# Optimization experiments

Hardware: AMD Instinct MI355X
Metric: run time of the kernel (lower is better)

## Reference

```python
import jax, jax.numpy as jnp
import numpy as np


def setup_inputs() -> dict:
    key = jax.random.key(0)
    kx, kw, kb = jax.random.split(key, 3)
    x = jax.random.normal(kx, (4, 2048, 4096), dtype=jnp.float32)
    weight = jax.random.normal(kw, (4096, 4096), dtype=jnp.float32) * 0.02
    bias = jax.random.normal(kb, (4096,), dtype=jnp.float32) * 0.02
    return {"x": x, "weight": weight, "bias": bias}


def _binarize_except_outliers(w):
    # Outlier mask from global weight stats (computed from w itself; in torch it
    # is cached after the first call but the values are identical every step).
    mean = jnp.mean(w)
    std = jnp.std(w, ddof=1)  # torch.std default is the unbiased estimator
    lower = mean - 1.96 * std
    upper = mean + 1.96 * std
    outliers = (w < lower) | (w > upper)
    keep = (~outliers).astype(w.dtype)
    # scaling_factor in the torch code: w[~outliers].abs().mean(-1) on the
    # flattened masked-select -> a single SCALAR, detached from the graph.
    scale = jax.lax.stop_gradient(jnp.sum(jnp.abs(w) * keep) / jnp.sum(keep))
    # NOTE: the torch code assigns STE-sign values and then immediately
    # overwrites them with w * scale, so the effective math is:
    w_bin = jnp.where(outliers, w, w * scale)
    return w_bin


def reference(x, weight, bias):
    w_bin = _binarize_except_outliers(weight)  # [out, in]
    # F.linear(x, w, b) = x @ w.T + b
    return jnp.einsum("bsi,oi->bso", x, w_bin) + bias
```

## Files before the change

### kernel.cpp

```cpp
#include <hip/hip_runtime.h>
#include <hip/hip_bf16.h>
#include <math.h>

#define MDIM 8192
#define NDIM 4096
#define KDIM 4096
#define WELEMS 16777216
#define XELEMS 33554432

typedef __attribute__((ext_vector_type(8))) short bf16x8;
typedef __attribute__((ext_vector_type(4))) float f32x4;

__device__ __forceinline__ unsigned short f2bf(float f) {
  unsigned int u = __float_as_uint(f);
  u += 0x7fffu + ((u >> 16) & 1u);
  return (unsigned short)(u >> 16);
}

__device__ __forceinline__ void gload16(const void* g, void* l) {
  __builtin_amdgcn_global_load_lds(
      (const __attribute__((address_space(1))) void*)g,
      (__attribute__((address_space(3))) void*)l, 16, 0, 0);
}

template <int MODE>
__global__ __launch_bounds__(256)
void np_stage1(const float* __restrict__ w, float* __restrict__ C,
               float* __restrict__ C2, const float* __restrict__ scal) {
  __shared__ float ls[32], ls2[32];
  const int t = threadIdx.x;
  const int leaf = t >> 3, j = t & 7;
  const size_t base = (size_t)blockIdx.x * 4096 + leaf * 128 + j;
  float mean = 0.f, lower = 0.f, upper = 0.f;
  if (MODE == 1) mean = scal[0];
  if (MODE == 2) { lower = scal[1]; upper = scal[2]; }
  float r = 0.f, r2 = 0.f;
#pragma unroll
  for (int s = 0; s < 16; s++) {
    float v = w[base + s * 8];
    float tv, tv2 = 0.f;
    if (MODE == 0) tv = v;
    else if (MODE == 1) { float x = v - mean; tv = __fmul_rn(x, x); }
    else {
      bool keep = !(v < lower || v > upper);
      tv = keep ? fabsf(v) : 0.f;
      tv2 = keep ? 1.f : 0.f;
    }
    if (s == 0) { r = tv; r2 = tv2; } else { r += tv; r2 += tv2; }
  }
  r += __shfl_xor(r, 1); r += __shfl_xor(r, 2); r += __shfl_xor(r, 4);
  if (MODE == 2) { r2 += __shfl_xor(r2, 1); r2 += __shfl_xor(r2, 2); r2 += __shfl_xor(r2, 4); }
  if (j == 0) { ls[leaf] = r; if (MODE == 2) ls2[leaf] = r2; }
  __syncthreads();
  if (t == 0) {
    float tmp[32];
    for (int i = 0; i < 32; i++) tmp[i] = ls[i];
    for (int n = 32; n > 1; n >>= 1)
      for (int i = 0; i < n / 2; i++) tmp[i] = tmp[2 * i] + tmp[2 * i + 1];
    C[blockIdx.x] = tmp[0];
    if (MODE == 2) {
      for (int i = 0; i < 32; i++) tmp[i] = ls2[i];
      for (int n = 32; n > 1; n >>= 1)
        for (int i = 0; i < n / 2; i++) tmp[i] = tmp[2 * i] + tmp[2 * i + 1];
      C2[blockIdx.x] = tmp[0];
    }
  }
}

template <int MODE>
__global__ __launch_bounds__(256)
void np_stage2(const float* __restrict__ C, const float* __restrict__ C2,
               float* __restrict__ scal) {
  __shared__ float ls[256], ls2[256];
  const int t = threadIdx.x;
  {
    float v[16];
    for (int i = 0; i < 16; i++) v[i] = C[t * 16 + i];
    for (int n = 16; n > 1; n >>= 1)
      for (int i = 0; i < n / 2; i++) v[i] = v[2 * i] + v[2 * i + 1];
    ls[t] = v[0];
    if (MODE == 2) {
      for (int i = 0; i < 16; i++) v[i] = C2[t * 16 + i];
      for (int n = 16; n > 1; n >>= 1)
        for (int i = 0; i < n / 2; i++) v[i] = v[2 * i] + v[2 * i + 1];
      ls2[t] = v[0];
    }
  }
  __syncthreads();
  if (t == 0) {
    float tmp[256];
    for (int i = 0; i < 256; i++) tmp[i] = ls[i];
    for (int n = 256; n > 1; n >>= 1)
      for (int i = 0; i < n / 2; i++) tmp[i] = tmp[2 * i] + tmp[2 * i + 1];
    float S = tmp[0];
    if (MODE == 0) {
      scal[0] = S / 16777216.0f;
    } else if (MODE == 1) {
      float var = S / 16777215.0f;
      float sd = sqrtf(var);
      float mean = scal[0];
      scal[1] = mean - __fmul_rn(1.96f, sd);
      scal[2] = mean + __fmul_rn(1.96f, sd);
    } else {
      for (int i = 0; i < 256; i++) tmp[i] = ls2[i];
      for (int n = 256; n > 1; n >>= 1)
        for (int i = 0; i < n / 2; i++) tmp[i] = tmp[2 * i] + tmp[2 * i + 1];
      scal[3] = S / tmp[0];
    }
  }
}

__device__ __forceinline__ void pack8(const float* __restrict__ p, unsigned short* dst,
                                      bool dobin, float lower, float upper, float scale) {
  float4 u = *(const float4*)p;
  float4 v = *(const float4*)(p + 4);
  float f[8] = {u.x, u.y, u.z, u.w, v.x, v.y, v.z, v.w};
  unsigned int r[4];
#pragma unroll
  for (int j = 0; j < 4; j++) {
    float a = f[2 * j], b = f[2 * j + 1];
    if (dobin) {
      bool oa = (a < lower) || (a > upper);
      bool ob = (b < lower) || (b > upper);
      a = oa ? a : __fmul_rn(a, scale);
      b = ob ? b : __fmul_rn(b, scale);
    }
    r[j] = (unsigned int)f2bf(a) | ((unsigned int)f2bf(b) << 16);
  }
  *(uint4*)dst = make_uint4(r[0], r[1], r[2], r[3]);
}

__global__ __launch_bounds__(256)
void convert_w(const float* __restrict__ w, unsigned short* __restrict__ wb,
               const float* __restrict__ scal) {
  float lower = scal[1], upper = scal[2], scale = scal[3];
  int tid = blockIdx.x * blockDim.x + threadIdx.x;
  int nth = gridDim.x * blockDim.x;
  int nc = WELEMS / 8;
  for (int i = tid; i < nc; i += nth)
    pack8(w + (size_t)i * 8, wb + (size_t)i * 8, true, lower, upper, scale);
}

__global__ __launch_bounds__(256)
void convert_x(const float* __restrict__ x, unsigned short* __restrict__ xb) {
  int tid = blockIdx.x * blockDim.x + threadIdx.x;
  int nth = gridDim.x * blockDim.x;
  int nc = XELEMS / 8;
  for (int i = tid; i < nc; i += nth)
    pack8(x + (size_t)i * 8, xb + (size_t)i * 8, false, 0.f, 0.f, 0.f);
}


#define VM(n) asm volatile("s_waitcnt vmcnt(" #n ")" ::: "memory")
#define PSYNC { asm volatile("" ::: "memory"); __builtin_amdgcn_s_barrier(); asm volatile("" ::: "memory"); }

#define RDA(slot, bufR, h) do { \
  slot[0][0] = *(const bf16x8*)&sA[bufR][wm][((2*(h)  )*16+fr)*64 + koo0]; \
  slot[0][1] = *(const bf16x8*)&sA[bufR][wm][((2*(h)  )*16+fr)*64 + koo1]; \
  slot[1][0] = *(const bf16x8*)&sA[bufR][wm][((2*(h)+1)*16+fr)*64 + koo0]; \
  slot[1][1] = *(const bf16x8*)&sA[bufR][wm][((2*(h)+1)*16+fr)*64 + koo1]; } while (0)

#define RDB2(slot, nf, bufR, bh) do { \
  slot[nf][0] = *(const bf16x8*)&sB[bufR][wnh][(wnq*64+(2*(bh)+(nf))*16+fr)*64 + koo0]; \
  slot[nf][1] = *(const bf16x8*)&sB[bufR][wnh][(wnq*64+(2*(bh)+(nf))*16+fr)*64 + koo1]; } while (0)

#define RDB4(slot, bufR, bh) do { RDB2(slot, 0, bufR, bh); RDB2(slot, 1, bufR, bh); } while (0)

#define MM8(AS, BSL, h, nh) do { \
  __builtin_amdgcn_s_setprio(1); \
  acc[2*(h)  ][2*(nh)  ] = __builtin_amdgcn_mfma_f32_16x16x32_bf16(AS[0][0], BSL[0][0], acc[2*(h)  ][2*(nh)  ], 0, 0, 0); \
  acc[2*(h)  ][2*(nh)+1] = __builtin_amdgcn_mfma_f32_16x16x32_bf16(AS[0][0], BSL[1][0], acc[2*(h)  ][2*(nh)+1], 0, 0, 0); \
  acc[2*(h)+1][2*(nh)  ] = __builtin_amdgcn_mfma_f32_16x16x32_bf16(AS[1][0], BSL[0][0], acc[2*(h)+1][2*(nh)  ], 0, 0, 0); \
  acc[2*(h)+1][2*(nh)+1] = __builtin_amdgcn_mfma_f32_16x16x32_bf16(AS[1][0], BSL[1][0], acc[2*(h)+1][2*(nh)+1], 0, 0, 0); \
  acc[2*(h)  ][2*(nh)  ] = __builtin_amdgcn_mfma_f32_16x16x32_bf16(AS[0][1], BSL[0][1], acc[2*(h)  ][2*(nh)  ], 0, 0, 0); \
  acc[2*(h)  ][2*(nh)+1] = __builtin_amdgcn_mfma_f32_16x16x32_bf16(AS[0][1], BSL[1][1], acc[2*(h)  ][2*(nh)+1], 0, 0, 0); \
  acc[2*(h)+1][2*(nh)  ] = __builtin_amdgcn_mfma_f32_16x16x32_bf16(AS[1][1], BSL[0][1], acc[2*(h)+1][2*(nh)  ], 0, 0, 0); \
  acc[2*(h)+1][2*(nh)+1] = __builtin_amdgcn_mfma_f32_16x16x32_bf16(AS[1][1], BSL[1][1], acc[2*(h)+1][2*(nh)+1], 0, 0, 0); \
  __builtin_amdgcn_s_setprio(0); } while (0)

#define STGA(buf, q, kadd) do { \
  gload16(xbp + aofA[0][q] + (kadd), &sA[buf][0][(q)*4096 + t8]); \
  gload16(xbp + aofA[1][q] + (kadd), &sA[buf][1][(q)*4096 + t8]); } while (0)
#define STGB(buf, h, kadd) do { \
  gload16(wbp + bofB[h][0] + (kadd), &sB[buf][h][t8]); \
  gload16(wbp + bofB[h][1] + (kadd), &sB[buf][h][4096 + t8]); } while (0)

#define TILE(BR, BW, BF, BS_, KADD) do { \
   PSYNC; RDB2(BS_, 0, BR, 1); STGA(BW, 0, KADD); MM8(aA, BF, 0, 0); \
   PSYNC; RDB2(BS_, 1, BR, 1); STGB(BW, 0, KADD); MM8(aB, BF, 1, 0); VM(4); \
   PSYNC; RDA(aC, BR, 2); STGB(BW, 1, KADD); MM8(aB, BS_, 1, 1); \
   PSYNC; RDA(aB, BR, 3); STGA(BW, 1, KADD); MM8(aA, BS_, 0, 1); \
   PSYNC; MM8(aC, BS_, 2, 1); VM(6); \
   PSYNC; RDA(aA, BW, 0); MM8(aB, BS_, 3, 1); VM(2); \
   PSYNC; MM8(aB, BF, 3, 0); RDB4(BS_, BW, 0); \
   PSYNC; MM8(aC, BF, 2, 0); RDA(aB, BW, 1); } while (0)

__global__ __launch_bounds__(512, 2)
void gemm256(const unsigned short* __restrict__ xbp, const unsigned short* __restrict__ wbp,
             const float* __restrict__ bias, float* __restrict__ out) {
  __shared__ unsigned short sA[2][2][8192];
  __shared__ unsigned short sB[2][2][8192];

  const int bid = blockIdx.x;
  const int swz = (bid & 7) * 64 + (bid >> 3);
  const int bm = swz >> 4, bn = swz & 15;

  const int t = threadIdx.x;
  const int lane = t & 63;
  const int wid = t >> 6;
  const int wm = wid >> 2, wn = wid & 3;
  const int wnh = wn >> 1, wnq = wn & 1;
  const int fr = lane & 15;
  const int ko = (lane >> 4) * 8;
  const int xr = (fr & 7) << 3;
  const int koo0 = ko ^ xr;
  const int koo1 = (32 + ko) ^ xr;

  const int t8 = t * 8;
  const int rl = t >> 3;
  const int cs = ((t & 7) * 8) ^ ((rl & 7) << 3);
  unsigned int aofA[2][2], bofB[2][2];
#pragma unroll
  for (int h = 0; h < 2; h++)
#pragma unroll
    for (int q = 0; q < 2; q++) {
      aofA[h][q] = (unsigned int)((bm * 256 + h * 128 + q * 64 + rl) * KDIM + cs);
      bofB[h][q] = (unsigned int)((bn * 256 + h * 128 + q * 64 + rl) * KDIM + cs);
    }

  f32x4 acc[8][4];
#pragma unroll
  for (int i = 0; i < 8; i++)
#pragma unroll
    for (int j = 0; j < 4; j++) acc[i][j] = {0.f, 0.f, 0.f, 0.f};

  bf16x8 aA[2][2], aB[2][2], aC[2][2], bs0[2][2], bs1[2][2];

  STGA(0, 0, 0); STGB(0, 0, 0); STGB(0, 1, 0); STGA(0, 1, 0);
  VM(2); PSYNC;
  RDA(aA, 0, 0); RDA(aB, 0, 1); RDB4(bs0, 0, 0);

  for (int it = 0; it < 31; ++it) {
    TILE(0, 1, bs0, bs1, 64);
    TILE(1, 0, bs1, bs0, 128);
#pragma unroll
    for (int h = 0; h < 2; h++)
#pragma unroll
      for (int q = 0; q < 2; q++) { aofA[h][q] += 128; bofB[h][q] += 128; }
  }
  TILE(0, 1, bs0, bs1, 64);
   PSYNC; RDB2(bs0, 0, 1, 1); MM8(aA, bs1, 0, 0);
   PSYNC; RDB2(bs0, 1, 1, 1); MM8(aB, bs1, 1, 0); VM(0);
   PSYNC; RDA(aC, 1, 2); MM8(aB, bs0, 1, 1);
   PSYNC; RDA(aB, 1, 3); MM8(aA, bs0, 0, 1);
   PSYNC; MM8(aC, bs0, 2, 1);
   PSYNC; MM8(aB, bs0, 3, 1);
   PSYNC; MM8(aB, bs1, 3, 0);
   PSYNC; MM8(aC, bs1, 2, 0);

#pragma unroll
  for (int nn = 0; nn < 4; ++nn) {
    const int col = bn * 256 + wn * 64 + nn * 16 + (lane & 15);
    const float bv = bias[col];
#pragma unroll
    for (int m = 0; m < 8; ++m) {
      const int row0 = bm * 256 + wm * 128 + m * 16 + (lane >> 4) * 4;
#pragma unroll
      for (int q = 0; q < 4; ++q)
        out[(size_t)(row0 + q) * NDIM + col] = acc[m][nn][q] + bv;
    }
  }
}

template <bool A_BF16, bool B_BF16>
__global__ __launch_bounds__(256)
void gemm_bt(const void* __restrict__ Av, const void* __restrict__ Bv,
             const float* __restrict__ bias, float* __restrict__ out,
             const float* __restrict__ scal) {
  __shared__ unsigned short sAt[2][128 * 32];
  __shared__ unsigned short sBt[2][128 * 32];
  float lower = 0.f, upper = 0.f, scale = 0.f;
  if constexpr (!B_BF16) { lower = scal[1]; upper = scal[2]; scale = scal[3]; }
  const unsigned short* Ab = (const unsigned short*)Av;
  const float* Af = (const float*)Av;
  const unsigned short* Bb = (const unsigned short*)Bv;
  const float* Bf = (const float*)Bv;
  int bid = blockIdx.x;
  int swz = (bid & 7) * 256 + (bid >> 3);
  int bm = swz >> 5, bn = swz & 31;
  const int t = threadIdx.x, lane = t & 63, wid = t >> 6;
  const int wm = wid >> 1, wn = wid & 1;
  const int e0 = t * 8, e1 = e0 + 2048;
  const size_t aOff0 = (size_t)(bm * 128 + (e0 >> 5)) * KDIM + (e0 & 31);
  const size_t aOff1 = (size_t)(bm * 128 + (e1 >> 5)) * KDIM + (e1 & 31);
  const size_t bOff0 = (size_t)(bn * 128 + (e0 >> 5)) * KDIM + (e0 & 31);
  const size_t bOff1 = (size_t)(bn * 128 + (e1 >> 5)) * KDIM + (e1 & 31);
  f32x4 acc[4][4];
#pragma unroll
  for (int i = 0; i < 4; i++)
#pragma unroll
    for (int j = 0; j < 4; j++) acc[i][j] = {0.f, 0.f, 0.f, 0.f};
  auto stage = [&](int buf, int k0) {
    if constexpr (A_BF16) {
      gload16(Ab + aOff0 + k0, &sAt[buf][e0]);
      gload16(Ab + aOff1 + k0, &sAt[buf][e1]);
    } else {
      pack8(Af + aOff0 + k0, &sAt[buf][e0], false, 0.f, 0.f, 0.f);
      pack8(Af + aOff1 + k0, &sAt[buf][e1], false, 0.f, 0.f, 0.f);
    }
    if constexpr (B_BF16) {
      gload16(Bb + bOff0 + k0, &sBt[buf][e0]);
      gload16(Bb + bOff1 + k0, &sBt[buf][e1]);
    } else {
      pack8(Bf + bOff0 + k0, &sBt[buf][e0], true, lower, upper, scale);
      pack8(Bf + bOff1 + k0, &sBt[buf][e1], true, lower, upper, scale);
    }
  };
  stage(0, 0);
  const int NT = KDIM / 32;
  const int ko = (lane >> 4) * 8, fr = lane & 15;
  for (int tt = 0; tt < NT; ++tt) {
    int cur = tt & 1;
    __syncthreads();
    if (tt + 1 < NT) stage(cur ^ 1, (tt + 1) * 32);
    bf16x8 a[4], b[4];
#pragma unroll
    for (int i = 0; i < 4; i++) {
      a[i] = *(const bf16x8*)&sAt[cur][(wm * 64 + i * 16 + fr) * 32 + ko];
      b[i] = *(const bf16x8*)&sBt[cur][(wn * 64 + i * 16 + fr) * 32 + ko];
    }
#pragma unroll
    for (int i = 0; i < 4; i++)
#pragma unroll
      for (int j = 0; j < 4; j++)
        acc[i][j] = __builtin_amdgcn_mfma_f32_16x16x32_bf16(a[i], b[j], acc[i][j], 0, 0, 0);
  }
  const int colbase = bn * 128 + wn * 64 + (lane & 15);
  const int rowbase = bm * 128 + wm * 64 + (lane >> 4) * 4;
#pragma unroll
  for (int j = 0; j < 4; j++) {
    int col = colbase + j * 16;
    float bv = bias[col];
#pragma unroll
    for (int i = 0; i < 4; i++) {
      int row0 = rowbase + i * 16;
#pragma unroll
      for (int q = 0; q < 4; q++)
        out[(size_t)(row0 + q) * NDIM + col] = acc[i][j][q] + bv;
    }
  }
}

extern "C" void kernel_launch(void* const* d_in, const int* in_sizes, int n_in,
                              void* d_out, int out_size, void* d_ws, size_t ws_size,
                              hipStream_t stream) {
  const float* x = (const float*)d_in[0];
  const float* w = (const float*)d_in[1];
  const float* bias = (const float*)d_in[2];
  float* out = (float*)d_out;
  char* ws = (char*)d_ws;

  const size_t xb_b = (size_t)XELEMS * 2;
  const size_t wb_b = (size_t)WELEMS * 2;
  const size_t c_b = 4 * 4096 * sizeof(float);
  const bool full = ws_size >= xb_b + wb_b + c_b + 64;
  const bool wonly = !full && ws_size >= wb_b + c_b + 64;

  unsigned short *xb = nullptr, *wb = nullptr;
  float *C1, *scal;
  if (full) {
    xb = (unsigned short*)ws;
    wb = (unsigned short*)(ws + xb_b);
    C1 = (float*)(ws + xb_b + wb_b);
  } else if (wonly) {
    wb = (unsigned short*)ws;
    C1 = (float*)(ws + wb_b);
  } else {
    C1 = (float*)ws;
  }
  float* C2 = C1 + 4096;
  float* C3 = C2 + 4096;
  float* C4 = C3 + 4096;
  scal = C4 + 4096;

  np_stage1<0><<<dim3(4096), dim3(256), 0, stream>>>(w, C1, nullptr, scal);
  np_stage2<0><<<dim3(1), dim3(256), 0, stream>>>(C1, nullptr, scal);
  np_stage1<1><<<dim3(4096), dim3(256), 0, stream>>>(w, C2, nullptr, scal);
  np_stage2<1><<<dim3(1), dim3(256), 0, stream>>>(C2, nullptr, scal);
  np_stage1<2><<<dim3(4096), dim3(256), 0, stream>>>(w, C3, C4, scal);
  np_stage2<2><<<dim3(1), dim3(256), 0, stream>>>(C3, C4, scal);

  if (full) {
    convert_w<<<dim3(2048), dim3(256), 0, stream>>>(w, wb, scal);
    convert_x<<<dim3(4096), dim3(256), 0, stream>>>(x, xb);
    gemm256<<<dim3(512), dim3(512), 0, stream>>>(xb, wb, bias, out);
  } else if (wonly) {
    convert_w<<<dim3(2048), dim3(256), 0, stream>>>(w, wb, scal);
    gemm_bt<false, true><<<dim3(2048), dim3(256), 0, stream>>>(x, wb, bias, out, scal);
  } else {
    gemm_bt<false, false><<<dim3(2048), dim3(256), 0, stream>>>(x, w, bias, out, scal);
  }
}
```

Before: 420.6 us.

## Fuse stat reductions with x conversion and load GEMM B operand from global

The full path drops the single-block stage2 reduction kernels. Each following kernel now redoes the small 4096-element partial-sum tree reduction itself, and the x-to-bf16 conversion runs as extra blocks inside the variance and keep-count kernels so it overlaps the weight statistics passes. The GEMM mainloop no longer stages B through LDS: each wave loads its B fragments straight from global memory into registers, LDS is halved, and the schedule becomes one barrier per K-step. The risk is redundant per-block reductions and uncoalesced or latency-exposed global B loads in the GEMM.

```diff
diff --git a/kernel.cpp b/kernel.cpp
--- a/kernel.cpp
+++ b/kernel.cpp
@@ -21,6 +21,30 @@
   __builtin_amdgcn_global_load_lds(
       (const __attribute__((address_space(1))) void*)g,
       (__attribute__((address_space(3))) void*)l, 16, 0, 0);
+}
+
+
+__device__ __forceinline__ float np_tree_reduce(const float* __restrict__ C, float* ls) {
+  const int t = threadIdx.x;
+  float v[16];
+#pragma unroll
+  for (int i = 0; i < 16; i++) v[i] = C[t * 16 + i];
+#pragma unroll
+  for (int n = 16; n > 1; n >>= 1)
+    for (int i = 0; i < n / 2; i++) v[i] = v[2 * i] + v[2 * i + 1];
+  __syncthreads();
+  ls[t] = v[0];
+  __syncthreads();
+  for (int n = 256; n > 1; n >>= 1) {
+    float s = 0.f;
+    if (t < n / 2) s = ls[2 * t] + ls[2 * t + 1];
+    __syncthreads();
+    if (t < n / 2) ls[t] = s;
+    __syncthreads();
+  }
+  float r = ls[0];
+  __syncthreads();
+  return r;
 }
 
 template <int MODE>
@@ -150,56 +174,171 @@
     pack8(x + (size_t)i * 8, xb + (size_t)i * 8, false, 0.f, 0.f, 0.f);
 }
 
-
-#define VM(n) asm volatile("s_waitcnt vmcnt(" #n ")" ::: "memory")
+__global__ __launch_bounds__(256)
+void k2_var_convx(const float* __restrict__ w, const float* __restrict__ x,
+                  const float* __restrict__ C1, float* __restrict__ C2,
+                  unsigned short* __restrict__ xb) {
+  if (blockIdx.x >= 4096) {
+    int bid2 = blockIdx.x - 4096;
+    for (int i = bid2 * 256 + threadIdx.x; i < XELEMS / 16; i += 2048 * 256)
+      pack8(x + (size_t)i * 8, xb + (size_t)i * 8, false, 0.f, 0.f, 0.f);
+    return;
+  }
+  __shared__ float red[256];
+  __shared__ float ls[32];
+  float mean = np_tree_reduce(C1, red) / 16777216.0f;
+  const int t = threadIdx.x;
+  const int leaf = t >> 3, j = t & 7;
+  const size_t base = (size_t)blockIdx.x * 4096 + leaf * 128 + j;
+  float r = 0.f;
+#pragma unroll
+  for (int s = 0; s < 16; s++) {
+    float v = w[base + s * 8];
+    float xv = v - mean;
+    float tv = __fmul_rn(xv, xv);
+    if (s == 0) r = tv; else r += tv;
+  }
+  r += __shfl_xor(r, 1); r += __shfl_xor(r, 2); r += __shfl_xor(r, 4);
+  if (j == 0) ls[leaf] = r;
+  __syncthreads();
+  if (t == 0) {
+    float tmp[32];
+    for (int i = 0; i < 32; i++) tmp[i] = ls[i];
+    for (int n = 32; n > 1; n >>= 1)
+      for (int i = 0; i < n / 2; i++) tmp[i] = tmp[2 * i] + tmp[2 * i + 1];
+    C2[blockIdx.x] = tmp[0];
+  }
+}
+
+__global__ __launch_bounds__(256)
+void k3_keep_convx(const float* __restrict__ w, const float* __restrict__ x,
+                   const float* __restrict__ C1, const float* __restrict__ C2,
+                   float* __restrict__ C3, float* __restrict__ C4,
+                   unsigned short* __restrict__ xb) {
+  if (blockIdx.x >= 4096) {
+    int bid2 = blockIdx.x - 4096;
+    for (int i = XELEMS / 16 + bid2 * 256 + threadIdx.x; i < XELEMS / 8; i += 2048 * 256)
+      pack8(x + (size_t)i * 8, xb + (size_t)i * 8, false, 0.f, 0.f, 0.f);
+    return;
+  }
+  __shared__ float red[256];
+  __shared__ float ls[32], ls2[32];
+  float S1 = np_tree_reduce(C1, red);
+  float S2 = np_tree_reduce(C2, red);
+  float mean = S1 / 16777216.0f;
+  float sd = sqrtf(S2 / 16777215.0f);
+  float lower = mean - __fmul_rn(1.96f, sd);
+  float upper = mean + __fmul_rn(1.96f, sd);
+  const int t = threadIdx.x;
+  const int leaf = t >> 3, j = t & 7;
+  const size_t base = (size_t)blockIdx.x * 4096 + leaf * 128 + j;
+  float r = 0.f, r2 = 0.f;
+#pragma unroll
+  for (int s = 0; s < 16; s++) {
+    float v = w[base + s * 8];
+    bool keep = !(v < lower || v > upper);
+    float tv = keep ? fabsf(v) : 0.f;
+    float tv2 = keep ? 1.f : 0.f;
+    if (s == 0) { r = tv; r2 = tv2; } else { r += tv; r2 += tv2; }
+  }
+  r += __shfl_xor(r, 1); r += __shfl_xor(r, 2); r += __shfl_xor(r, 4);
+  r2 += __shfl_xor(r2, 1); r2 += __shfl_xor(r2, 2); r2 += __shfl_xor(r2, 4);
+  if (j == 0) { ls[leaf] = r; ls2[leaf] = r2; }
+  __syncthreads();
+  if (t == 0) {
+    float tmp[32];
+    for (int i = 0; i < 32; i++) tmp[i] = ls[i];
+    for (int n = 32; n > 1; n >>= 1)
+      for (int i = 0; i < n / 2; i++) tmp[i] = tmp[2 * i] + tmp[2 * i + 1];
+    C3[blockIdx.x] = tmp[0];
+    for (int i = 0; i < 32; i++) tmp[i] = ls2[i];
+    for (int n = 32; n > 1; n >>= 1)
+      for (int i = 0; i < n / 2; i++) tmp[i] = tmp[2 * i] + tmp[2 * i + 1];
+    C4[blockIdx.x] = tmp[0];
+  }
+}
+
+__global__ __launch_bounds__(256)
+void k4_convw(const float* __restrict__ w, const float* __restrict__ C1,
+              const float* __restrict__ C2, const float* __restrict__ C3,
+              const float* __restrict__ C4, unsigned short* __restrict__ wb) {
+  __shared__ float red[256];
+  float S1 = np_tree_reduce(C1, red);
+  float S2 = np_tree_reduce(C2, red);
+  float S3 = np_tree_reduce(C3, red);
+  float S4 = np_tree_reduce(C4, red);
+  float mean = S1 / 16777216.0f;
+  float sd = sqrtf(S2 / 16777215.0f);
+  float lower = mean - __fmul_rn(1.96f, sd);
+  float upper = mean + __fmul_rn(1.96f, sd);
+  float scale = S3 / S4;
+  int tid = blockIdx.x * blockDim.x + threadIdx.x;
+  int nth = gridDim.x * blockDim.x;
+  int nc = WELEMS / 8;
+  for (int i = tid; i < nc; i += nth)
+    pack8(w + (size_t)i * 8, wb + (size_t)i * 8, true, lower, upper, scale);
+}
+
+
+#define VM8 asm volatile("s_waitcnt vmcnt(8)" ::: "memory")
 #define PSYNC { asm volatile("" ::: "memory"); __builtin_amdgcn_s_barrier(); asm volatile("" ::: "memory"); }
 
-#define RDA(slot, bufR, h) do { \
-  slot[0][0] = *(const bf16x8*)&sA[bufR][wm][((2*(h)  )*16+fr)*64 + koo0]; \
-  slot[0][1] = *(const bf16x8*)&sA[bufR][wm][((2*(h)  )*16+fr)*64 + koo1]; \
-  slot[1][0] = *(const bf16x8*)&sA[bufR][wm][((2*(h)+1)*16+fr)*64 + koo0]; \
-  slot[1][1] = *(const bf16x8*)&sA[bufR][wm][((2*(h)+1)*16+fr)*64 + koo1]; } while (0)
-
-#define RDB2(slot, nf, bufR, bh) do { \
-  slot[nf][0] = *(const bf16x8*)&sB[bufR][wnh][(wnq*64+(2*(bh)+(nf))*16+fr)*64 + koo0]; \
-  slot[nf][1] = *(const bf16x8*)&sB[bufR][wnh][(wnq*64+(2*(bh)+(nf))*16+fr)*64 + koo1]; } while (0)
-
-#define RDB4(slot, bufR, bh) do { RDB2(slot, 0, bufR, bh); RDB2(slot, 1, bufR, bh); } while (0)
-
-#define MM8(AS, BSL, h, nh) do { \
+#define RDAQ(slot, bufR, mh) do { \
+  slot[0][0] = *(const bf16x8*)&sA[bufR][wm][((mh)*64 +  0 + fr)*64 + koo0]; \
+  slot[0][1] = *(const bf16x8*)&sA[bufR][wm][((mh)*64 +  0 + fr)*64 + koo1]; \
+  slot[1][0] = *(const bf16x8*)&sA[bufR][wm][((mh)*64 + 16 + fr)*64 + koo0]; \
+  slot[1][1] = *(const bf16x8*)&sA[bufR][wm][((mh)*64 + 16 + fr)*64 + koo1]; \
+  slot[2][0] = *(const bf16x8*)&sA[bufR][wm][((mh)*64 + 32 + fr)*64 + koo0]; \
+  slot[2][1] = *(const bf16x8*)&sA[bufR][wm][((mh)*64 + 32 + fr)*64 + koo1]; \
+  slot[3][0] = *(const bf16x8*)&sA[bufR][wm][((mh)*64 + 48 + fr)*64 + koo0]; \
+  slot[3][1] = *(const bf16x8*)&sA[bufR][wm][((mh)*64 + 48 + fr)*64 + koo1]; } while (0)
+
+#define LDBG(dst, nh, kadd) do { \
+  dst[0][0] = *(const bf16x8*)(wbp + bofR[nh][0] + (kadd)); \
+  dst[0][1] = *(const bf16x8*)(wbp + bofR[nh][0] + (kadd) + 32); \
+  dst[1][0] = *(const bf16x8*)(wbp + bofR[nh][1] + (kadd)); \
+  dst[1][1] = *(const bf16x8*)(wbp + bofR[nh][1] + (kadd) + 32); } while (0)
+
+#define MM1(m, n, ks, AS, BS) acc[m][n] = __builtin_amdgcn_mfma_f32_16x16x32_bf16(AS[(m)&3][ks], BS[(n)&1][ks], acc[m][n], 0, 0, 0)
+#define MMQ(mh, nh, AS, BS) do { \
   __builtin_amdgcn_s_setprio(1); \
-  acc[2*(h)  ][2*(nh)  ] = __builtin_amdgcn_mfma_f32_16x16x32_bf16(AS[0][0], BSL[0][0], acc[2*(h)  ][2*(nh)  ], 0, 0, 0); \
-  acc[2*(h)  ][2*(nh)+1] = __builtin_amdgcn_mfma_f32_16x16x32_bf16(AS[0][0], BSL[1][0], acc[2*(h)  ][2*(nh)+1], 0, 0, 0); \
-  acc[2*(h)+1][2*(nh)  ] = __builtin_amdgcn_mfma_f32_16x16x32_bf16(AS[1][0], BSL[0][0], acc[2*(h)+1][2*(nh)  ], 0, 0, 0); \
-  acc[2*(h)+1][2*(nh)+1] = __builtin_amdgcn_mfma_f32_16x16x32_bf16(AS[1][0], BSL[1][0], acc[2*(h)+1][2*(nh)+1], 0, 0, 0); \
-  acc[2*(h)  ][2*(nh)  ] = __builtin_amdgcn_mfma_f32_16x16x32_bf16(AS[0][1], BSL[0][1], acc[2*(h)  ][2*(nh)  ], 0, 0, 0); \
-  acc[2*(h)  ][2*(nh)+1] = __builtin_amdgcn_mfma_f32_16x16x32_bf16(AS[0][1], BSL[1][1], acc[2*(h)  ][2*(nh)+1], 0, 0, 0); \
-  acc[2*(h)+1][2*(nh)  ] = __builtin_amdgcn_mfma_f32_16x16x32_bf16(AS[1][1], BSL[0][1], acc[2*(h)+1][2*(nh)  ], 0, 0, 0); \
-  acc[2*(h)+1][2*(nh)+1] = __builtin_amdgcn_mfma_f32_16x16x32_bf16(AS[1][1], BSL[1][1], acc[2*(h)+1][2*(nh)+1], 0, 0, 0); \
+  MM1((mh)*4+0, (nh)*2+0, 0, AS, BS); MM1((mh)*4+0, (nh)*2+1, 0, AS, BS); \
+  MM1((mh)*4+1, (nh)*2+0, 0, AS, BS); MM1((mh)*4+1, (nh)*2+1, 0, AS, BS); \
+  MM1((mh)*4+2, (nh)*2+0, 0, AS, BS); MM1((mh)*4+2, (nh)*2+1, 0, AS, BS); \
+  MM1((mh)*4+3, (nh)*2+0, 0, AS, BS); MM1((mh)*4+3, (nh)*2+1, 0, AS, BS); \
+  MM1((mh)*4+0, (nh)*2+0, 1, AS, BS); MM1((mh)*4+0, (nh)*2+1, 1, AS, BS); \
+  MM1((mh)*4+1, (nh)*2+0, 1, AS, BS); MM1((mh)*4+1, (nh)*2+1, 1, AS, BS); \
+  MM1((mh)*4+2, (nh)*2+0, 1, AS, BS); MM1((mh)*4+2, (nh)*2+1, 1, AS, BS); \
+  MM1((mh)*4+3, (nh)*2+0, 1, AS, BS); MM1((mh)*4+3, (nh)*2+1, 1, AS, BS); \
   __builtin_amdgcn_s_setprio(0); } while (0)
 
 #define STGA(buf, q, kadd) do { \
   gload16(xbp + aofA[0][q] + (kadd), &sA[buf][0][(q)*4096 + t8]); \
   gload16(xbp + aofA[1][q] + (kadd), &sA[buf][1][(q)*4096 + t8]); } while (0)
-#define STGB(buf, h, kadd) do { \
-  gload16(wbp + bofB[h][0] + (kadd), &sB[buf][h][t8]); \
-  gload16(wbp + bofB[h][1] + (kadd), &sB[buf][h][4096 + t8]); } while (0)
-
-#define TILE(BR, BW, BF, BS_, KADD) do { \
-   PSYNC; RDB2(BS_, 0, BR, 1); STGA(BW, 0, KADD); MM8(aA, BF, 0, 0); \
-   PSYNC; RDB2(BS_, 1, BR, 1); STGB(BW, 0, KADD); MM8(aB, BF, 1, 0); VM(4); \
-   PSYNC; RDA(aC, BR, 2); STGB(BW, 1, KADD); MM8(aB, BS_, 1, 1); \
-   PSYNC; RDA(aB, BR, 3); STGA(BW, 1, KADD); MM8(aA, BS_, 0, 1); \
-   PSYNC; MM8(aC, BS_, 2, 1); VM(6); \
-   PSYNC; RDA(aA, BW, 0); MM8(aB, BS_, 3, 1); VM(2); \
-   PSYNC; MM8(aB, BF, 3, 0); RDB4(BS_, BW, 0); \
-   PSYNC; MM8(aC, BF, 2, 0); RDA(aB, BW, 1); } while (0)
+
+#define BUMP64 do { \
+  aofA[0][0] += 64; aofA[0][1] += 64; aofA[1][0] += 64; aofA[1][1] += 64; \
+  bofR[0][0] += 64; bofR[0][1] += 64; bofR[1][0] += 64; bofR[1][1] += 64; } while (0)
+
+#define TILE(CUR, NXT) do { \
+  PSYNC; \
+  RDAQ(aP, CUR, 0); \
+  STGA(NXT, 0, 64); STGA(NXT, 1, 64); \
+  MMQ(0, 0, aP, bN0); \
+  RDAQ(aQ, CUR, 1); \
+  MMQ(1, 0, aQ, bN0); \
+  LDBG(bN0, 0, 64); \
+  MMQ(1, 1, aQ, bN1); \
+  MMQ(0, 1, aP, bN1); \
+  LDBG(bN1, 1, 64); \
+  VM8; \
+  BUMP64; \
+} while (0)
 
 __global__ __launch_bounds__(512, 2)
 void gemm256(const unsigned short* __restrict__ xbp, const unsigned short* __restrict__ wbp,
              const float* __restrict__ bias, float* __restrict__ out) {
   __shared__ unsigned short sA[2][2][8192];
-  __shared__ unsigned short sB[2][2][8192];
 
   const int bid = blockIdx.x;
   const int swz = (bid & 7) * 64 + (bid >> 3);
@@ -219,14 +358,19 @@
   const int t8 = t * 8;
   const int rl = t >> 3;
   const int cs = ((t & 7) * 8) ^ ((rl & 7) << 3);
-  unsigned int aofA[2][2], bofB[2][2];
+  unsigned int aofA[2][2];
 #pragma unroll
   for (int h = 0; h < 2; h++)
 #pragma unroll
-    for (int q = 0; q < 2; q++) {
+    for (int q = 0; q < 2; q++)
       aofA[h][q] = (unsigned int)((bm * 256 + h * 128 + q * 64 + rl) * KDIM + cs);
-      bofB[h][q] = (unsigned int)((bn * 256 + h * 128 + q * 64 + rl) * KDIM + cs);
-    }
+
+  unsigned int bofR[2][2];
+#pragma unroll
+  for (int nh = 0; nh < 2; nh++)
+#pragma unroll
+    for (int nf = 0; nf < 2; nf++)
+      bofR[nh][nf] = (unsigned int)((bn * 256 + wnh * 128 + wnq * 64 + nh * 32 + nf * 16 + fr) * KDIM + ko);
 
   f32x4 acc[8][4];
 #pragma unroll
@@ -234,29 +378,24 @@
 #pragma unroll
     for (int j = 0; j < 4; j++) acc[i][j] = {0.f, 0.f, 0.f, 0.f};
 
-  bf16x8 aA[2][2], aB[2][2], aC[2][2], bs0[2][2], bs1[2][2];
-
-  STGA(0, 0, 0); STGB(0, 0, 0); STGB(0, 1, 0); STGA(0, 1, 0);
-  VM(2); PSYNC;
-  RDA(aA, 0, 0); RDA(aB, 0, 1); RDB4(bs0, 0, 0);
+  bf16x8 aP[4][2], aQ[4][2], bN0[2][2], bN1[2][2];
+
+  STGA(0, 0, 0); STGA(0, 1, 0);
+  LDBG(bN0, 0, 0); LDBG(bN1, 1, 0);
+  VM8;
 
   for (int it = 0; it < 31; ++it) {
-    TILE(0, 1, bs0, bs1, 64);
-    TILE(1, 0, bs1, bs0, 128);
-#pragma unroll
-    for (int h = 0; h < 2; h++)
-#pragma unroll
-      for (int q = 0; q < 2; q++) { aofA[h][q] += 128; bofB[h][q] += 128; }
-  }
-  TILE(0, 1, bs0, bs1, 64);
-   PSYNC; RDB2(bs0, 0, 1, 1); MM8(aA, bs1, 0, 0);
-   PSYNC; RDB2(bs0, 1, 1, 1); MM8(aB, bs1, 1, 0); VM(0);
-   PSYNC; RDA(aC, 1, 2); MM8(aB, bs0, 1, 1);
-   PSYNC; RDA(aB, 1, 3); MM8(aA, bs0, 0, 1);
-   PSYNC; MM8(aC, bs0, 2, 1);
-   PSYNC; MM8(aB, bs0, 3, 1);
-   PSYNC; MM8(aB, bs1, 3, 0);
-   PSYNC; MM8(aC, bs1, 2, 0);
+    TILE(0, 1);
+    TILE(1, 0);
+  }
+  TILE(0, 1);
+  PSYNC;
+  RDAQ(aP, 1, 0);
+  MMQ(0, 0, aP, bN0);
+  RDAQ(aQ, 1, 1);
+  MMQ(1, 0, aQ, bN0);
+  MMQ(1, 1, aQ, bN1);
+  MMQ(0, 1, aP, bN1);
 
 #pragma unroll
   for (int nn = 0; nn < 4; ++nn) {
@@ -383,21 +522,24 @@
   float* C4 = C3 + 4096;
   scal = C4 + 4096;
 
-  np_stage1<0><<<dim3(4096), dim3(256), 0, stream>>>(w, C1, nullptr, scal);
-  np_stage2<0><<<dim3(1), dim3(256), 0, stream>>>(C1, nullptr, scal);
-  np_stage1<1><<<dim3(4096), dim3(256), 0, stream>>>(w, C2, nullptr, scal);
-  np_stage2<1><<<dim3(1), dim3(256), 0, stream>>>(C2, nullptr, scal);
-  np_stage1<2><<<dim3(4096), dim3(256), 0, stream>>>(w, C3, C4, scal);
-  np_stage2<2><<<dim3(1), dim3(256), 0, stream>>>(C3, C4, scal);
-
   if (full) {
-    convert_w<<<dim3(2048), dim3(256), 0, stream>>>(w, wb, scal);
-    convert_x<<<dim3(4096), dim3(256), 0, stream>>>(x, xb);
+    np_stage1<0><<<dim3(4096), dim3(256), 0, stream>>>(w, C1, nullptr, scal);
+    k2_var_convx<<<dim3(6144), dim3(256), 0, stream>>>(w, x, C1, C2, xb);
+    k3_keep_convx<<<dim3(6144), dim3(256), 0, stream>>>(w, x, C1, C2, C3, C4, xb);
+    k4_convw<<<dim3(2048), dim3(256), 0, stream>>>(w, C1, C2, C3, C4, wb);
     gemm256<<<dim3(512), dim3(512), 0, stream>>>(xb, wb, bias, out);
-  } else if (wonly) {
-    convert_w<<<dim3(2048), dim3(256), 0, stream>>>(w, wb, scal);
-    gemm_bt<false, true><<<dim3(2048), dim3(256), 0, stream>>>(x, wb, bias, out, scal);
   } else {
-    gemm_bt<false, false><<<dim3(2048), dim3(256), 0, stream>>>(x, w, bias, out, scal);
-  }
-}
+    np_stage1<0><<<dim3(4096), dim3(256), 0, stream>>>(w, C1, nullptr, scal);
+    np_stage2<0><<<dim3(1), dim3(256), 0, stream>>>(C1, nullptr, scal);
+    np_stage1<1><<<dim3(4096), dim3(256), 0, stream>>>(w, C2, nullptr, scal);
+    np_stage2<1><<<dim3(1), dim3(256), 0, stream>>>(C2, nullptr, scal);
+    np_stage1<2><<<dim3(4096), dim3(256), 0, stream>>>(w, C3, C4, scal);
+    np_stage2<2><<<dim3(1), dim3(256), 0, stream>>>(C3, C4, scal);
+    if (wonly) {
+      convert_w<<<dim3(2048), dim3(256), 0, stream>>>(w, wb, scal);
+      gemm_bt<false, true><<<dim3(2048), dim3(256), 0, stream>>>(x, wb, bias, out, scal);
+    } else {
+      gemm_bt<false, false><<<dim3(2048), dim3(256), 0, stream>>>(x, w, bias, out, scal);
+    }
+  }
+}
```

After: 531.7 us. 1.26x slower.
